# Kernel optimization log

Measured on AMD Instinct MI355X. Metric: run time of the kernel, lower is better.

## Reference

```python
import jax, jax.numpy as jnp
import numpy as np
import math

NUM_HEADS = 16
EMBED_DIM = 1024
DIM_HEAD = EMBED_DIM // NUM_HEADS


def setup_inputs() -> dict:
    key = jax.random.key(0)
    k_x, k_wi, k_bi, k_wo, k_bo = jax.random.split(key, 5)
    B, S, D = 2, 2048, EMBED_DIM
    scale = 1.0 / math.sqrt(D)
    return {
        "x": jax.random.normal(k_x, (B, S, D), dtype=jnp.float32),
        "w_in": jax.random.normal(k_wi, (3 * D, D), dtype=jnp.float32) * scale,
        "b_in": jax.random.normal(k_bi, (3 * D,), dtype=jnp.float32) * 0.02,
        "w_out": jax.random.normal(k_wo, (D, D), dtype=jnp.float32) * scale,
        "b_out": jax.random.normal(k_bo, (D,), dtype=jnp.float32) * 0.02,
    }


def reference(x, w_in, b_in, w_out, b_out):
    B, S, D = x.shape
    H, Dh = NUM_HEADS, DIM_HEAD
    # in_proj: x @ w_in.T + b_in -> chunk into q, k, v
    qkv = jnp.einsum("bsd,ed->bse", x, w_in) + b_in  # [B,S,3D]
    q, k, v = jnp.split(qkv, 3, axis=-1)
    q = q.reshape(B, S, H, Dh).transpose(0, 2, 1, 3)  # [B,H,S,Dh]
    k = k.reshape(B, S, H, Dh).transpose(0, 2, 1, 3)
    v = v.reshape(B, S, H, Dh).transpose(0, 2, 1, 3)
    # scores, causal mask (masked_fill before scaling == after, since -inf/c = -inf)
    scores = jnp.einsum("bhqd,bhkd->bhqk", q, k) / math.sqrt(Dh)
    causal = jnp.triu(jnp.ones((S, S), dtype=bool), k=1)
    scores = jnp.where(causal, -jnp.inf, scores)
    weight = jax.nn.softmax(scores, axis=-1)
    out = jnp.einsum("bhqk,bhkd->bhqd", weight, v)  # [B,H,S,Dh]
    out = out.transpose(0, 2, 1, 3).reshape(B, S, D)
    return jnp.einsum("bsd,ed->bse", out, w_out) + b_out
```

## Files before the change

### kernel.cpp

```cpp
#include <hip/hip_runtime.h>
#include <stdint.h>

typedef unsigned short u16;
typedef float f32x4 __attribute__((ext_vector_type(4)));
typedef __bf16 bf16x8 __attribute__((ext_vector_type(8)));

#define AS1 __attribute__((address_space(1)))
#define AS3 __attribute__((address_space(3)))

#define QK_SCALE 0.18033688011112042f

__device__ __forceinline__ u16 f32_to_bf16(float f) {
    unsigned u = __float_as_uint(f);
    unsigned r = u + 0x7fffu + ((u >> 16) & 1u);
    return (u16)(r >> 16);
}

__device__ __forceinline__ float bf16_f(u16 u) {
    return __uint_as_float(((unsigned)u) << 16);
}

__device__ __forceinline__ void gload_lds16(const u16* g, u16* l) {
    __builtin_amdgcn_global_load_lds((const AS1 unsigned int*)g,
                                     (AS3 unsigned int*)l, 16, 0, 0);
}

__device__ __forceinline__ int swz(int row, int col8) {
    return row * 64 + (((col8 ^ (row & 7)) & 7) << 3);
}
__device__ __forceinline__ int swzv(int row, int col8) {
    return row * 64 + (((col8 ^ row ^ (row >> 3)) & 7) << 3);
}

__global__ __launch_bounds__(256) void cvt_bf16_3(const float4* __restrict__ in0,
                                                  const float4* __restrict__ in1,
                                                  const float4* __restrict__ in2,
                                                  uint2* __restrict__ out,
                                                  int n0, int n1, int ntot) {
    for (int i = blockIdx.x * blockDim.x + threadIdx.x; i < ntot;
         i += gridDim.x * blockDim.x) {
        float4 v;
        if (i < n0) v = in0[i];
        else if (i < n0 + n1) {
            v = in1[i - n0];
            if (((i - n0) >> 8) < 1024) {
                v.x *= QK_SCALE; v.y *= QK_SCALE; v.z *= QK_SCALE; v.w *= QK_SCALE;
            }
        } else v = in2[i - n0 - n1];
        uint2 o;
        o.x = (unsigned)f32_to_bf16(v.x) | ((unsigned)f32_to_bf16(v.y) << 16);
        o.y = (unsigned)f32_to_bf16(v.z) | ((unsigned)f32_to_bf16(v.w) << 16);
        out[i] = o;
    }
}

template <int BNT, bool BF16_OUT>
__global__ __launch_bounds__(512, 2) void gemm_ring(const u16* __restrict__ A,
                                                    const u16* __restrict__ B,
                                                    const float* __restrict__ bias,
                                                    void* __restrict__ Cv,
                                                    int M, int N, int K,
                                                    int qcols, float qscale) {
    extern __shared__ u16 lds[];
    constexpr int NACC = BNT / 64;
    constexpr int NCH = (128 + BNT) >> 7;
    constexpr int ASZ = 128 * 32;
    constexpr int BSZ = BNT * 32;
    const int t = threadIdx.x;
    const int l = t & 63, w = t >> 6;
    const int lr = l & 15, lhi = l >> 4;
    const int wm = w >> 2, wn = w & 3;
    const int orig = blockIdx.y * gridDim.x + blockIdx.x;
    const int sid = (orig & 7) * 32 + (orig >> 3);
    const int bm = sid & 31, bn = sid >> 5;

    const u16* Ag = A + (size_t)bm * 128 * K;
    const u16* Bg = B + (size_t)bn * BNT * K;

    auto STAGE = [&](int kt, int slot) {
        u16* As = lds + slot * ASZ;
        u16* Bs = lds + 4 * ASZ + slot * BSZ;
        {
            int c = t, row = c >> 2, cp = c & 3;
            int gc = (cp ^ ((row >> 1) & 3)) << 3;
            gload_lds16(Ag + (size_t)row * K + kt * 32 + gc, As + c * 8);
        }
        #pragma unroll
        for (int i = 0; i < NCH - 1; ++i) {
            int c = i * 512 + t, row = c >> 2, cp = c & 3;
            int gc = (cp ^ ((row >> 1) & 3)) << 3;
            gload_lds16(Bg + (size_t)row * K + kt * 32 + gc, Bs + c * 8);
        }
    };

    f32x4 acc[4][NACC] = {};
    const int NT = K >> 5;
    STAGE(0, 0);
    STAGE(1, 1);
    STAGE(2, 2);

    const int ckey = (lr >> 1) & 3;

    for (int kt = 0; kt < NT; ++kt) {
        if (kt < NT - 2) {
            if constexpr (NCH == 4) asm volatile("s_waitcnt vmcnt(8)" ::: "memory");
            else                    asm volatile("s_waitcnt vmcnt(4)" ::: "memory");
        } else if (kt == NT - 2) {
            if constexpr (NCH == 4) asm volatile("s_waitcnt vmcnt(4)" ::: "memory");
            else                    asm volatile("s_waitcnt vmcnt(2)" ::: "memory");
        } else {
            asm volatile("s_waitcnt vmcnt(0)" ::: "memory");
        }
        __builtin_amdgcn_s_barrier();

        if (kt + 3 < NT) STAGE(kt + 3, (kt + 3) & 3);

        const u16* As = lds + (kt & 3) * ASZ;
        const u16* Bs = lds + 4 * ASZ + (kt & 3) * BSZ;
        bf16x8 af[4], bfv[NACC];
        #pragma unroll
        for (int m = 0; m < 4; ++m) {
            int row = wm * 64 + m * 16 + lr;
            af[m] = *(const bf16x8*)(As + row * 32 + ((lhi ^ ckey) << 3));
        }
        #pragma unroll
        for (int n = 0; n < NACC; ++n) {
            int row = wn * (BNT / 4) + n * 16 + lr;
            bfv[n] = *(const bf16x8*)(Bs + row * 32 + ((lhi ^ ckey) << 3));
        }
        asm volatile("s_waitcnt lgkmcnt(0)" ::: "memory");
        __builtin_amdgcn_sched_barrier(0);
        __builtin_amdgcn_s_setprio(1);
        #pragma unroll
        for (int m = 0; m < 4; ++m)
            #pragma unroll
            for (int n = 0; n < NACC; ++n)
                acc[m][n] = __builtin_amdgcn_mfma_f32_16x16x32_bf16(
                    af[m], bfv[n], acc[m][n], 0, 0, 0);
        __builtin_amdgcn_s_setprio(0);
    }

    const int row0 = bm * 128 + wm * 64 + lhi * 4;
    const int col0 = bn * BNT + wn * (BNT / 4) + lr;
    #pragma unroll
    for (int n = 0; n < NACC; ++n) {
        int col = col0 + n * 16;
        float bv = bias[col];
        if (col < qcols) bv *= qscale;
        #pragma unroll
        for (int m = 0; m < 4; ++m)
            #pragma unroll
            for (int r = 0; r < 4; ++r) {
                int row = row0 + m * 16 + r;
                float v = acc[m][n][r] + bv;
                if constexpr (BF16_OUT)
                    ((u16*)Cv)[(size_t)row * N + col] = f32_to_bf16(v);
                else
                    ((float*)Cv)[(size_t)row * N + col] = v;
            }
    }
}

__device__ __forceinline__ void write_vt(u16* vt, uint4 a, uint4 b, int g, int cl) {
    unsigned aw[4] = {a.x, a.y, a.z, a.w};
    unsigned bw[4] = {b.x, b.y, b.z, b.w};
    #pragma unroll
    for (int j = 0; j < 8; ++j) {
        int dh = cl * 8 + j;
        unsigned sel = (j & 1) ? 0x07060302u : 0x05040100u;
        unsigned v = __builtin_amdgcn_perm(bw[j >> 1], aw[j >> 1], sel);
        *(unsigned*)(vt + swzv(dh, g >> 2) + (2 * g & 7)) = v;
    }
}

__global__ __launch_bounds__(512, 4) void attn_kernel(const u16* __restrict__ qkv,
                                                      u16* __restrict__ out) {
    extern __shared__ u16 alds[];
    const int t = threadIdx.x;
    const int w = t >> 6, l = t & 63;
    const int lr = l & 15, lhi = l >> 4;
    const int par = w >> 2, wl = w & 3;
    const int tp = t & 255;
    const int orig = blockIdx.x;
    const int sid = (orig & 7) * 64 + (orig >> 3);
    const int bh = sid >> 4, bi = sid & 15;
    const int h = bh & 15, b = bh >> 4;

    const u16* Kg = qkv + ((size_t)(b * 2048)) * 3072 + 1024 + h * 64;
    const u16* Vg = qkv + ((size_t)(b * 2048)) * 3072 + 2048 + h * 64;
    const int vg = tp >> 3, vcl = tp & 7;
    u16* KsP = alds + par * 8192;
    u16* VtP = alds + 16384 + par * 8192;
    u16* Pw = alds + 32768 + w * 1024;
    unsigned* Pst = (unsigned*)Pw;
    float2* mlX = (float2*)alds;

    #pragma unroll 1
    for (int pass = 0; pass < 2; ++pass) {
        const int qt = pass ? (31 - bi) : bi;
        __syncthreads();

        const u16* Qrow = qkv + ((size_t)(b * 2048 + qt * 64 + wl * 16 + lr)) * 3072 + h * 64;
        bf16x8 qf0 = *(const bf16x8*)(Qrow + lhi * 8);
        bf16x8 qf1 = *(const bf16x8*)(Qrow + 32 + lhi * 8);

        uint4 va = {0, 0, 0, 0}, vbr = {0, 0, 0, 0};
        if (par <= qt) {
            #pragma unroll
            for (int i = 0; i < 2; ++i) {
                int c = i * 256 + tp, r = c >> 3, cl = c & 7;
                gload_lds16(Kg + ((size_t)(par * 64 + r)) * 3072 + ((cl ^ (r & 7)) << 3),
                            KsP + c * 8);
            }
            va = *(const uint4*)(Vg + ((size_t)(par * 64 + 2 * vg)) * 3072 + vcl * 8);
            vbr = *(const uint4*)(Vg + ((size_t)(par * 64 + 2 * vg + 1)) * 3072 + vcl * 8);
            write_vt(VtP, va, vbr, vg, vcl);
        }
        __syncthreads();

        f32x4 acc[4] = {};
        float m_run = -1e30f, l_run = 0.f;
        int cur = 0;
        const int nt = (qt >> 1) + 1;

        for (int it = 0; it < nt; ++it) {
            const int t64 = 2 * it + par;
            const bool active = (t64 <= qt);
            const bool pf = (t64 + 2 <= qt);
            if (pf) {
                #pragma unroll
                for (int i = 0; i < 2; ++i) {
                    int c = i * 256 + tp, r = c >> 3, cl = c & 7;
                    gload_lds16(Kg + ((size_t)((t64 + 2) * 64 + r)) * 3072 +
                                    ((cl ^ (r & 7)) << 3),
                                KsP + (cur ^ 1) * 4096 + c * 8);
                }
                va = *(const uint4*)(Vg + ((size_t)((t64 + 2) * 64 + 2 * vg)) * 3072 + vcl * 8);
                vbr = *(const uint4*)(Vg + ((size_t)((t64 + 2) * 64 + 2 * vg + 1)) * 3072 + vcl * 8);
            }

            f32x4 sv[4] = {};
            if (active) {
                const u16* Kc = KsP + cur * 4096;
                __builtin_amdgcn_s_setprio(1);
                #pragma unroll
                for (int kks = 0; kks < 2; ++kks) {
                    #pragma unroll
                    for (int n = 0; n < 4; ++n) {
                        bf16x8 kf = *(const bf16x8*)(Kc + swz(n * 16 + lr, kks * 4 + lhi));
                        sv[n] = __builtin_amdgcn_mfma_f32_16x16x32_bf16(
                            kf, kks ? qf1 : qf0, sv[n], 0, 0, 0);
                    }
                }
                __builtin_amdgcn_s_setprio(0);

                if (t64 == qt) {
                    #pragma unroll
                    for (int n = 0; n < 4; ++n)
                        #pragma unroll
                        for (int r = 0; r < 4; ++r)
                            if ((n * 16 + lhi * 4 + r) > (wl * 16 + lr)) sv[n][r] = -1e30f;
                }
                float t0 = fmaxf(fmaxf(sv[0][0], sv[0][1]), fmaxf(sv[0][2], sv[0][3]));
                float t1 = fmaxf(fmaxf(sv[1][0], sv[1][1]), fmaxf(sv[1][2], sv[1][3]));
                float t2 = fmaxf(fmaxf(sv[2][0], sv[2][1]), fmaxf(sv[2][2], sv[2][3]));
                float t3 = fmaxf(fmaxf(sv[3][0], sv[3][1]), fmaxf(sv[3][2], sv[3][3]));
                float mx = fmaxf(fmaxf(t0, t1), fmaxf(t2, t3));
                mx = fmaxf(mx, __shfl_xor(mx, 16, 64));
                mx = fmaxf(mx, __shfl_xor(mx, 32, 64));

                if (__any(mx > m_run + 8.f)) {
                    float mn = fmaxf(m_run, mx);
                    float alpha = exp2f(m_run - mn);
                    m_run = mn;
                    l_run *= alpha;
                    #pragma unroll
                    for (int r = 0; r < 4; ++r) {
                        float ar = __shfl(alpha, lhi * 4 + r, 16);
                        #pragma unroll
                        for (int n = 0; n < 4; ++n) acc[n][r] *= ar;
                    }
                }

                float rs = 0.f;
                #pragma unroll
                for (int n = 0; n < 4; ++n)
                    #pragma unroll
                    for (int r = 0; r < 4; ++r) {
                        float pe = exp2f(sv[n][r] - m_run);
                        sv[n][r] = pe;
                        rs += pe;
                    }
                l_run += rs;

                #pragma unroll
                for (int n = 0; n < 4; ++n)
                    #pragma unroll
                    for (int rp = 0; rp < 2; ++rp) {
                        union { unsigned u; __bf16 hh[2]; } pk;
                        pk.hh[0] = (__bf16)sv[n][2 * rp];
                        pk.hh[1] = (__bf16)sv[n][2 * rp + 1];
                        int pp = 8 * n + 2 * lhi + rp;
                        Pst[lr * 32 + (((pp >> 2) ^ (lr & 7)) << 2) + (pp & 3)] = pk.u;
                    }
            }

            if (pf) write_vt(VtP + (cur ^ 1) * 4096, va, vbr, vg, vcl);

            if (active) {
                const u16* Vc = VtP + cur * 4096;
                __builtin_amdgcn_s_setprio(1);
                #pragma unroll
                for (int kks = 0; kks < 2; ++kks) {
                    bf16x8 pa = *(const bf16x8*)(Pw + lr * 64 +
                                                 (((kks * 4 + lhi) ^ (lr & 7)) << 3));
                    #pragma unroll
                    for (int n = 0; n < 4; ++n) {
                        bf16x8 vb = *(const bf16x8*)(Vc + swzv(n * 16 + lr, kks * 4 + lhi));
                        acc[n] = __builtin_amdgcn_mfma_f32_16x16x32_bf16(pa, vb, acc[n], 0, 0, 0);
                    }
                }
                __builtin_amdgcn_s_setprio(0);
            }

            __syncthreads();
            cur ^= 1;
        }

        l_run += __shfl_xor(l_run, 16, 64);
        l_run += __shfl_xor(l_run, 32, 64);

        if (par == 1) {
            if (lhi == 0) mlX[wl * 16 + lr] = make_float2(m_run, l_run);
            #pragma unroll
            for (int r = 0; r < 4; ++r)
                #pragma unroll
                for (int n = 0; n < 4; ++n)
                    Pw[(lhi * 4 + r) * 64 + n * 16 + lr] = f32_to_bf16(acc[n][r]);
        }
        __syncthreads();
        if (par == 0) {
            float2 m1l1 = mlX[wl * 16 + lr];
            float m = fmaxf(m_run, m1l1.x);
            float e0 = exp2f(m_run - m), e1 = exp2f(m1l1.x - m);
            float inv = 1.0f / (l_run * e0 + m1l1.y * e1);
            float c0 = e0 * inv, c1 = e1 * inv;
            const u16* Pq = alds + 32768 + (4 + wl) * 1024;
            #pragma unroll
            for (int r = 0; r < 4; ++r) {
                float c0r = __shfl(c0, lhi * 4 + r, 16);
                float c1r = __shfl(c1, lhi * 4 + r, 16);
                int qg = qt * 64 + wl * 16 + lhi * 4 + r;
                size_t base = ((size_t)(b * 2048 + qg)) * 1024 + h * 64;
                #pragma unroll
                for (int n = 0; n < 4; ++n) {
                    float v1 = bf16_f(Pq[(lhi * 4 + r) * 64 + n * 16 + lr]);
                    out[base + n * 16 + lr] = f32_to_bf16(acc[n][r] * c0r + v1 * c1r);
                }
            }
        }
    }
}

extern "C" void kernel_launch(void* const* d_in, const int* in_sizes, int n_in,
                              void* d_out, int out_size, void* d_ws, size_t ws_size,
                              hipStream_t stream) {
    const float* x = (const float*)d_in[0];
    const float* w_in = (const float*)d_in[1];
    const float* b_in = (const float*)d_in[2];
    const float* w_out = (const float*)d_in[3];
    const float* b_out = (const float*)d_in[4];
    float* out = (float*)d_out;

    u16* xb = (u16*)d_ws;
    u16* wib = xb + (size_t)4096 * 1024;
    u16* wob = wib + (size_t)3072 * 1024;
    u16* qkvb = wob + (size_t)1024 * 1024;
    u16* attnb = qkvb + (size_t)4096 * 3072;

    const int n0 = 4096 * 1024 / 4, n1 = 3072 * 1024 / 4, n2 = 1024 * 1024 / 4;
    cvt_bf16_3<<<2048, 256, 0, stream>>>((const float4*)x, (const float4*)w_in,
                                         (const float4*)w_out, (uint2*)xb,
                                         n0, n1, n0 + n1 + n2);

    (void)hipFuncSetAttribute((const void*)gemm_ring<384, true>,
                              hipFuncAttributeMaxDynamicSharedMemorySize, 131072);
    (void)hipFuncSetAttribute((const void*)gemm_ring<128, false>,
                              hipFuncAttributeMaxDynamicSharedMemorySize, 65536);
    (void)hipFuncSetAttribute((const void*)attn_kernel,
                              hipFuncAttributeMaxDynamicSharedMemorySize, 81920);

    gemm_ring<384, true><<<dim3(32, 8), 512, 131072, stream>>>(
        xb, wib, b_in, qkvb, 4096, 3072, 1024, 1024, QK_SCALE);
    attn_kernel<<<512, 512, 81920, stream>>>(qkvb, attnb);
    gemm_ring<128, false><<<dim3(32, 8), 512, 65536, stream>>>(
        attnb, wob, b_out, out, 4096, 1024, 1024, 0, 1.0f);
}
```

Measured before the change: 109.3 us.

## Single-buffer V tile in static LDS, add barrier, relax GEMM waitcnt

The attention kernel moves from dynamic to static shared memory and single-buffers the transposed V tile. The V write for the next tile now happens after an extra __syncthreads that follows the PV MFMAs, which cuts LDS use from 80KB to 64KB and may allow more blocks per CU. The cost is an additional block-wide barrier per iteration. In the GEMM, the explicit lgkmcnt(0) wait and sched_barrier before the MFMAs are replaced by a sched_barrier right after s_barrier, letting the compiler interleave LDS reads with MFMAs.

```diff
diff --git a/kernel.cpp b/kernel.cpp
--- a/kernel.cpp
+++ b/kernel.cpp
@@ -112,6 +112,7 @@
             asm volatile("s_waitcnt vmcnt(0)" ::: "memory");
         }
         __builtin_amdgcn_s_barrier();
+        __builtin_amdgcn_sched_barrier(0);
 
         if (kt + 3 < NT) STAGE(kt + 3, (kt + 3) & 3);
 
@@ -128,8 +129,6 @@
             int row = wn * (BNT / 4) + n * 16 + lr;
             bfv[n] = *(const bf16x8*)(Bs + row * 32 + ((lhi ^ ckey) << 3));
         }
-        asm volatile("s_waitcnt lgkmcnt(0)" ::: "memory");
-        __builtin_amdgcn_sched_barrier(0);
         __builtin_amdgcn_s_setprio(1);
         #pragma unroll
         for (int m = 0; m < 4; ++m)
@@ -175,7 +174,9 @@
 
 __global__ __launch_bounds__(512, 4) void attn_kernel(const u16* __restrict__ qkv,
                                                       u16* __restrict__ out) {
-    extern __shared__ u16 alds[];
+    __shared__ u16 Ks[2][2][64 * 64];
+    __shared__ u16 Vt[2][64 * 64];
+    __shared__ u16 Ps[8][16 * 64];
     const int t = threadIdx.x;
     const int w = t >> 6, l = t & 63;
     const int lr = l & 15, lhi = l >> 4;
@@ -189,11 +190,9 @@
     const u16* Kg = qkv + ((size_t)(b * 2048)) * 3072 + 1024 + h * 64;
     const u16* Vg = qkv + ((size_t)(b * 2048)) * 3072 + 2048 + h * 64;
     const int vg = tp >> 3, vcl = tp & 7;
-    u16* KsP = alds + par * 8192;
-    u16* VtP = alds + 16384 + par * 8192;
-    u16* Pw = alds + 32768 + w * 1024;
+    u16* Pw = Ps[w];
     unsigned* Pst = (unsigned*)Pw;
-    float2* mlX = (float2*)alds;
+    float2* mlX = (float2*)&Ks[0][0][0];
 
     #pragma unroll 1
     for (int pass = 0; pass < 2; ++pass) {
@@ -210,11 +209,11 @@
             for (int i = 0; i < 2; ++i) {
                 int c = i * 256 + tp, r = c >> 3, cl = c & 7;
                 gload_lds16(Kg + ((size_t)(par * 64 + r)) * 3072 + ((cl ^ (r & 7)) << 3),
-                            KsP + c * 8);
+                            &Ks[par][0][c * 8]);
             }
             va = *(const uint4*)(Vg + ((size_t)(par * 64 + 2 * vg)) * 3072 + vcl * 8);
             vbr = *(const uint4*)(Vg + ((size_t)(par * 64 + 2 * vg + 1)) * 3072 + vcl * 8);
-            write_vt(VtP, va, vbr, vg, vcl);
+            write_vt(Vt[par], va, vbr, vg, vcl);
         }
         __syncthreads();
 
@@ -226,28 +225,27 @@
         for (int it = 0; it < nt; ++it) {
             const int t64 = 2 * it + par;
             const bool active = (t64 <= qt);
-            const bool pf = (t64 + 2 <= qt);
-            if (pf) {
+            const bool pfv = (t64 + 2 <= qt);
+            if (pfv) {
                 #pragma unroll
                 for (int i = 0; i < 2; ++i) {
                     int c = i * 256 + tp, r = c >> 3, cl = c & 7;
                     gload_lds16(Kg + ((size_t)((t64 + 2) * 64 + r)) * 3072 +
                                     ((cl ^ (r & 7)) << 3),
-                                KsP + (cur ^ 1) * 4096 + c * 8);
+                                &Ks[par][cur ^ 1][c * 8]);
                 }
                 va = *(const uint4*)(Vg + ((size_t)((t64 + 2) * 64 + 2 * vg)) * 3072 + vcl * 8);
                 vbr = *(const uint4*)(Vg + ((size_t)((t64 + 2) * 64 + 2 * vg + 1)) * 3072 + vcl * 8);
             }
 
-            f32x4 sv[4] = {};
             if (active) {
-                const u16* Kc = KsP + cur * 4096;
+                f32x4 sv[4] = {};
                 __builtin_amdgcn_s_setprio(1);
                 #pragma unroll
                 for (int kks = 0; kks < 2; ++kks) {
                     #pragma unroll
                     for (int n = 0; n < 4; ++n) {
-                        bf16x8 kf = *(const bf16x8*)(Kc + swz(n * 16 + lr, kks * 4 + lhi));
+                        bf16x8 kf = *(const bf16x8*)(&Ks[par][cur][swz(n * 16 + lr, kks * 4 + lhi)]);
                         sv[n] = __builtin_amdgcn_mfma_f32_16x16x32_bf16(
                             kf, kks ? qf1 : qf0, sv[n], 0, 0, 0);
                     }
@@ -303,12 +301,7 @@
                         int pp = 8 * n + 2 * lhi + rp;
                         Pst[lr * 32 + (((pp >> 2) ^ (lr & 7)) << 2) + (pp & 3)] = pk.u;
                     }
-            }
-
-            if (pf) write_vt(VtP + (cur ^ 1) * 4096, va, vbr, vg, vcl);
-
-            if (active) {
-                const u16* Vc = VtP + cur * 4096;
+
                 __builtin_amdgcn_s_setprio(1);
                 #pragma unroll
                 for (int kks = 0; kks < 2; ++kks) {
@@ -316,13 +309,15 @@
                                                  (((kks * 4 + lhi) ^ (lr & 7)) << 3));
                     #pragma unroll
                     for (int n = 0; n < 4; ++n) {
-                        bf16x8 vb = *(const bf16x8*)(Vc + swzv(n * 16 + lr, kks * 4 + lhi));
+                        bf16x8 vb = *(const bf16x8*)(&Vt[par][swzv(n * 16 + lr, kks * 4 + lhi)]);
                         acc[n] = __builtin_amdgcn_mfma_f32_16x16x32_bf16(pa, vb, acc[n], 0, 0, 0);
                     }
                 }
                 __builtin_amdgcn_s_setprio(0);
             }
 
+            __syncthreads();
+            if (pfv) write_vt(Vt[par], va, vbr, vg, vcl);
             __syncthreads();
             cur ^= 1;
         }
@@ -345,7 +340,7 @@
             float e0 = exp2f(m_run - m), e1 = exp2f(m1l1.x - m);
             float inv = 1.0f / (l_run * e0 + m1l1.y * e1);
             float c0 = e0 * inv, c1 = e1 * inv;
-            const u16* Pq = alds + 32768 + (4 + wl) * 1024;
+            const u16* Pq = Ps[4 + wl];
             #pragma unroll
             for (int r = 0; r < 4; ++r) {
                 float c0r = __shfl(c0, lhi * 4 + r, 16);
@@ -387,12 +382,10 @@
                               hipFuncAttributeMaxDynamicSharedMemorySize, 131072);
     (void)hipFuncSetAttribute((const void*)gemm_ring<128, false>,
                               hipFuncAttributeMaxDynamicSharedMemorySize, 65536);
-    (void)hipFuncSetAttribute((const void*)attn_kernel,
-                              hipFuncAttributeMaxDynamicSharedMemorySize, 81920);
 
     gemm_ring<384, true><<<dim3(32, 8), 512, 131072, stream>>>(
         xb, wib, b_in, qkvb, 4096, 3072, 1024, 1024, QK_SCALE);
-    attn_kernel<<<512, 512, 81920, stream>>>(qkvb, attnb);
+    attn_kernel<<<512, 512, 0, stream>>>(qkvb, attnb);
     gemm_ring<128, false><<<dim3(32, 8), 512, 65536, stream>>>(
         attnb, wob, b_out, out, 4096, 1024, 1024, 0, 1.0f);
 }
```

Result: faster. 105.4 us (-3.6%).
